# Optimization experiments

Measured on AMD Instinct MI355X. Metric: run time of the kernel, lower is better.

The kernel has to match this reference:

```python
import jax, jax.numpy as jnp
import numpy as np

N = 100000      # nodes
E = 800000      # edges (before self-loops)
G = 128         # graphs
IN = 64         # per-table embedding dim (6 tables -> 384 input features)
L = 128         # layer_embd
OUT = 128       # out_embd
H = 2           # attention heads (concat=False -> mean over heads)
VOCABS = [33, 5, 3, 4, 2, 3]
NEG_SLOPE = 0.2
BN_EPS = 1e-5


def _seg_softmax(logits, seg, n):
    # softmax of per-edge/per-node logits grouped by segment id
    m = jax.ops.segment_max(logits, seg, num_segments=n)
    e = jnp.exp(logits - m[seg])
    s = jax.ops.segment_sum(e, seg, num_segments=n)
    return e / (s[seg] + 1e-16)


def _gat_conv(x, W, a_src, a_dst, b, src, dst, n):
    # PyG GATConv, add_self_loops already applied to (src,dst), concat=False
    h = (x @ W).reshape(n, H, -1)                 # [N,H,C]
    al_s = jnp.sum(h * a_src, axis=-1)            # [N,H]
    al_d = jnp.sum(h * a_dst, axis=-1)            # [N,H]
    e = jax.nn.leaky_relu(al_s[src] + al_d[dst], NEG_SLOPE)   # [E,H]
    alpha = _seg_softmax(e, dst, n)               # softmax over each dst's in-edges
    msg = h[src] * alpha[:, :, None]              # [E,H,C]
    out = jax.ops.segment_sum(msg, dst, num_segments=n)       # [N,H,C]
    return out.mean(axis=1) + b                   # head-mean + bias


def setup_inputs() -> dict:
    key = jax.random.key(0)
    ks = jax.random.split(key, 40)
    cols = [jax.random.randint(ks[i], (N, 1), 0, VOCABS[i]) for i in range(6)]
    x = jnp.concatenate(cols, axis=1).astype(jnp.int64)
    edge_index = jax.random.randint(ks[6], (2, E), 0, N).astype(jnp.int64)
    edge_type = jax.random.randint(ks[7], (E,), 0, 4).astype(jnp.int64)
    batch = jnp.sort(jax.random.randint(ks[8], (N,), 0, G)).astype(jnp.int64)
    s = 0.05
    p = {}
    for i in range(6):
        p[f"emb{i}"] = jax.random.normal(ks[10 + i], (VOCABS[i], IN)) * s
    p["W1"] = jax.random.normal(ks[16], (6 * IN, H * L)) * s
    p["as1"] = jax.random.normal(ks[17], (H, L)) * s
    p["ad1"] = jax.random.normal(ks[18], (H, L)) * s
    p["b1"] = jnp.zeros((L,))
    p["W2"] = jax.random.normal(ks[19], (L, H * OUT)) * s
    p["as2"] = jax.random.normal(ks[20], (H, OUT)) * s
    p["ad2"] = jax.random.normal(ks[21], (H, OUT)) * s
    p["b2"] = jnp.zeros((OUT,))
    p["gw1"] = jax.random.normal(ks[22], (OUT, OUT)) * s
    p["gb1"] = jnp.zeros((OUT,))
    p["bn_g"] = jnp.ones((OUT,))
    p["bn_b"] = jnp.zeros((OUT,))
    p["bn_m"] = jnp.zeros((OUT,))
    p["bn_v"] = jnp.ones((OUT,))
    p["gw2"] = jax.random.normal(ks[23], (OUT, 1)) * s
    p["gb2"] = jnp.zeros((1,))
    p["glw"] = jax.random.normal(ks[24], (OUT, 1)) * s
    p["glb"] = jnp.zeros((1,))
    return dict(x=x, edge_index=edge_index, edge_type=edge_type, batch=batch, **p)


def reference(x, edge_index, edge_type, batch,
              emb0, emb1, emb2, emb3, emb4, emb5,
              W1, as1, ad1, b1, W2, as2, ad2, b2,
              gw1, gb1, bn_g, bn_b, bn_m, bn_v, gw2, gb2, glw, glb):
    n = x.shape[0]
    embs = [emb0, emb1, emb2, emb3, emb4, emb5]
    x_ = jnp.concatenate([embs[i][x[:, i]] for i in range(6)], axis=1)  # [N, 6*IN]
    loops = jnp.arange(n)
    src = jnp.concatenate([edge_index[0], loops])
    dst = jnp.concatenate([edge_index[1], loops])
    out = jax.nn.sigmoid(_gat_conv(x_, W1, as1, ad1, b1, src, dst, n))
    out = jax.nn.sigmoid(_gat_conv(out, W2, as2, ad2, b2, src, dst, n))
    # GlobalAttention pooling (eval-mode BatchNorm in gate_nn)
    gh = out @ gw1 + gb1
    gh = (gh - bn_m) / jnp.sqrt(bn_v + BN_EPS) * bn_g + bn_b
    gh = jax.nn.relu(gh)
    logits = gh @ gw2 + gb2                       # [N,1]
    gate = _seg_softmax(logits, batch, G)         # softmax over nodes per graph
    pooled = jax.ops.segment_sum(gate * out, batch, num_segments=G)  # [G,OUT]
    return jax.nn.sigmoid(pooled @ glw + glb)     # [G,1]
```

## Files before the change

### kernel.cpp

```cpp
#include <hip/hip_runtime.h>
#include <hip/hip_bf16.h>
#include <hip/hip_fp16.h>

#define NN 100000
#define EE 800000
#define GG 128

typedef short bf16x8 __attribute__((ext_vector_type(8)));
typedef float f32x4 __attribute__((ext_vector_type(4)));
typedef float f32x2 __attribute__((ext_vector_type(2)));

__device__ __forceinline__ float bf2f(unsigned short v) {
    union { unsigned int u; float f; } x; x.u = ((unsigned int)v) << 16; return x.f;
}
__device__ __forceinline__ unsigned short f2bf(float f) {
    union { float f; unsigned int u; } x; x.f = f;
    unsigned int r = x.u + 0x7fffu + ((x.u >> 16) & 1u);
    return (unsigned short)(r >> 16);
}
__device__ __forceinline__ float sigmoidf_(float x) { return 1.f / (1.f + __expf(-x)); }
__device__ __forceinline__ float ldp(const void* p, int i, int f) {
    return f ? ((const float*)p)[i] : bf2f(((const unsigned short*)p)[i]);
}

#if defined(__has_builtin)
#if __has_builtin(__builtin_amdgcn_cvt_pk_f32_fp8) && __has_builtin(__builtin_amdgcn_cvt_pk_fp8_f32)
#define USE_HW_FP8 1
#endif
#endif
#ifndef USE_HW_FP8
#define USE_HW_FP8 0
#endif

#if USE_HW_FP8
__device__ __forceinline__ int fp8_pack2(float a, float b) {
    return __builtin_amdgcn_cvt_pk_fp8_f32(a, b, 0, false);
}
__device__ __forceinline__ void fp8_dec4(unsigned int q, float& f0, float& f1, float& f2, float& f3) {
    f32x2 lo = __builtin_amdgcn_cvt_pk_f32_fp8((int)q, false);
    f32x2 hi = __builtin_amdgcn_cvt_pk_f32_fp8((int)q, true);
    f0 = lo.x; f1 = lo.y; f2 = hi.x; f3 = hi.y;
}
#else
__device__ __forceinline__ unsigned char f2bf8(float f) {
    unsigned short u = __half_as_ushort(__float2half(f));
    unsigned short r = u + 0x7f + ((u >> 8) & 1);
    return (unsigned char)(r >> 8);
}
__device__ __forceinline__ int fp8_pack2(float a, float b) {
    return (int)f2bf8(a) | ((int)f2bf8(b) << 8);
}
__device__ __forceinline__ float bf8_dec(unsigned int b) {
    return __half2float(__ushort_as_half((unsigned short)(b << 8)));
}
__device__ __forceinline__ void fp8_dec4(unsigned int q, float& f0, float& f1, float& f2, float& f3) {
    f0 = bf8_dec(q & 0xff); f1 = bf8_dec((q >> 8) & 0xff);
    f2 = bf8_dec((q >> 16) & 0xff); f3 = bf8_dec(q >> 24);
}
#endif

__global__ void k_probe2(const unsigned int* __restrict__ w, const int* __restrict__ ei,
                         int* __restrict__ fflag, int* __restrict__ iflag) {
    __shared__ int s[256];
    int t = threadIdx.x;
    if (blockIdx.x == 0) {
        int cnt = 0;
        for (int i = t; i < 1024; i += 256) {
            unsigned int v = w[i];
            int e = (v >> 7) & 0xff;
            cnt += (e >= 100 && e <= 127) ? 1 : 0;
        }
        s[t] = cnt; __syncthreads();
        for (int d = 128; d > 0; d >>= 1) { if (t < d) s[t] += s[t + d]; __syncthreads(); }
        if (t == 0) fflag[0] = (s[0] >= 512) ? 0 : 1;
    } else {
        int nz = 0;
        for (int i = t; i < 1024; i += 256) nz |= ei[2 * i + 1];
        s[t] = nz; __syncthreads();
        for (int d = 128; d > 0; d >>= 1) { if (t < d) s[t] |= s[t + d]; __syncthreads(); }
        if (t == 0) iflag[0] = (s[0] == 0) ? 1 : 0;
    }
}

__global__ void k_cvt(const int* __restrict__ xi, const int* __restrict__ ei,
                      const int* __restrict__ bi, const int* __restrict__ flag,
                      int* __restrict__ xn, int* __restrict__ srcn,
                      int* __restrict__ dstn, int* __restrict__ batchn,
                      int* __restrict__ count) {
    int j = blockIdx.x * 256 + threadIdx.x;
    int f = flag[0];
    const int XT = NN * 6, ET = 2 * EE;
    if (j < XT) xn[j] = f ? xi[2 * j] : xi[j];
    int je = j - XT;
    if (je >= 0 && je < ET) {
        int v = f ? ei[2 * je] : ei[je];
        if (je < EE) srcn[je] = v;
        else { dstn[je - EE] = v; atomicAdd(&count[v], 1); }
    }
    int jb = j - XT - ET;
    if (jb >= 0 && jb < NN) batchn[jb] = f ? bi[2 * jb] : bi[jb];
}

__global__ void k_chunk_sum(const int* __restrict__ count, int* __restrict__ csum) {
    __shared__ int s[256];
    int t = threadIdx.x;
    int base = blockIdx.x * 1024 + t * 4;
    int acc = 0;
    #pragma unroll
    for (int j = 0; j < 4; j++) { int n = base + j; if (n < NN) acc += count[n]; }
    s[t] = acc; __syncthreads();
    for (int d = 128; d > 0; d >>= 1) { if (t < d) s[t] += s[t + d]; __syncthreads(); }
    if (t == 0) csum[blockIdx.x] = s[0];
}

__global__ void k_chunk_scan(const int* __restrict__ csum, int* __restrict__ coff, int nchunk) {
    __shared__ int s[256];
    int t = threadIdx.x;
    int v = (t < nchunk) ? csum[t] : 0;
    s[t] = v; __syncthreads();
    for (int d = 1; d < 256; d <<= 1) {
        int x = (t >= d) ? s[t - d] : 0;
        __syncthreads(); s[t] += x; __syncthreads();
    }
    if (t < nchunk) coff[t] = s[t] - v;
}

__global__ void k_scan_write(const int* __restrict__ count, const int* __restrict__ coff,
                             int* __restrict__ offset, int* __restrict__ cursor) {
    __shared__ int s[256];
    int t = threadIdx.x;
    int base = blockIdx.x * 1024 + t * 4;
    int v[4]; int acc = 0;
    #pragma unroll
    for (int j = 0; j < 4; j++) { v[j] = (base + j < NN) ? count[base + j] : 0; acc += v[j]; }
    s[t] = acc; __syncthreads();
    for (int d = 1; d < 256; d <<= 1) {
        int x = (t >= d) ? s[t - d] : 0;
        __syncthreads(); s[t] += x; __syncthreads();
    }
    int pre = s[t] - acc + coff[blockIdx.x];
    #pragma unroll
    for (int j = 0; j < 4; j++) {
        if (base + j < NN) { offset[base + j] = pre; cursor[base + j] = pre; pre += v[j]; }
    }
}

__global__ void k_scatter(const int* __restrict__ src, const int* __restrict__ dst,
                          int* __restrict__ cursor, int2* __restrict__ esrt) {
    int e = blockIdx.x * 256 + threadIdx.x;
    if (e < EE) {
        int d = dst[e];
        int p = atomicAdd(&cursor[d], 1);
        esrt[p] = make_int2(src[e], d);
    }
}

__global__ void k_cvtp(const void* e0, const void* e1, const void* e2,
                       const void* e3, const void* e4, const void* e5,
                       const void* W1, const void* W2,
                       const void* as1, const void* ad1, const void* b1,
                       const void* as2, const void* ad2, const void* b2,
                       const void* gw1, const void* gb1,
                       const void* bng, const void* bnb, const void* bnm, const void* bnv,
                       const void* gw2, const void* gb2, const void* glw, const void* glb,
                       const int* __restrict__ fflag,
                       unsigned short* __restrict__ embc,
                       unsigned short* __restrict__ W1T, unsigned short* __restrict__ W2T,
                       unsigned short* __restrict__ GWT, float* __restrict__ gb1p,
                       float* __restrict__ vs1, float* __restrict__ vd1,
                       float* __restrict__ vs2, float* __restrict__ vd2,
                       float* __restrict__ vb1, float* __restrict__ vb2,
                       float* __restrict__ gw2f, float* __restrict__ glwf,
                       float* __restrict__ gb2f, float* __restrict__ glbf) {
    int i = blockIdx.x * 256 + threadIdx.x;
    int f = fflag[0];
    if (i < 98304) { int k = i / 256, n = i % 256; W1T[n * 384 + k] = f2bf(ldp(W1, i, f)); }
    if (i < 32768) { int k = i / 256, n = i % 256; W2T[n * 128 + k] = f2bf(ldp(W2, i, f)); }
    if (i < 16384) {
        int n = i >> 7, k = i & 127;
        float sc = ldp(bng, n, f) * rsqrtf(ldp(bnv, n, f) + 1e-5f);
        GWT[i] = f2bf(ldp(gw1, k * 128 + n, f) * sc);
    }
    if (i < 3200) {
        const void* src; int base;
        if (i < 2112)      { src = e0; base = 0; }
        else if (i < 2432) { src = e1; base = 2112; }
        else if (i < 2624) { src = e2; base = 2432; }
        else if (i < 2880) { src = e3; base = 2624; }
        else if (i < 3008) { src = e4; base = 2880; }
        else               { src = e5; base = 3008; }
        embc[i] = f2bf(ldp(src, i - base, f));
    }
    if (i < 256) {
        vs1[i] = ldp(as1, i, f); vd1[i] = ldp(ad1, i, f);
        vs2[i] = ldp(as2, i, f); vd2[i] = ldp(ad2, i, f);
    }
    if (i < 128) {
        vb1[i] = ldp(b1, i, f); vb2[i] = ldp(b2, i, f);
        gw2f[i] = ldp(gw2, i, f); glwf[i] = ldp(glw, i, f);
        float sc = ldp(bng, i, f) * rsqrtf(ldp(bnv, i, f) + 1e-5f);
        gb1p[i] = (ldp(gb1, i, f) - ldp(bnm, i, f)) * sc + ldp(bnb, i, f);
    }
    if (i == 0) { gb2f[0] = ldp(gb2, 0, f); glbf[0] = ldp(glb, 0, f); }
}

__global__ __launch_bounds__(256, 2) void k_gemm(
    const unsigned short* __restrict__ Ain, const int* __restrict__ xidx,
    const unsigned short* __restrict__ embc,
    const unsigned short* __restrict__ WT, unsigned char* __restrict__ H8,
    const float* __restrict__ avs, const float* __restrict__ avd,
    float* __restrict__ alS, float* __restrict__ alD,
    int K, int mode)
{
    __shared__ __align__(16) unsigned short As[128 * 32];
    __shared__ __align__(16) unsigned short Bs[256 * 32];
    const int tab_base[6] = {0, 2112, 2432, 2624, 2880, 3008};
    int tid = threadIdx.x;
    int wave = tid >> 6, lane = tid & 63;
    int quad = lane >> 4, lr = lane & 15;
    int m0 = blockIdx.x * 128;

    f32x4 zero4 = {0.f, 0.f, 0.f, 0.f};
    f32x4 acc[2][16];
    #pragma unroll
    for (int i = 0; i < 2; i++)
        #pragma unroll
        for (int j = 0; j < 16; j++) acc[i][j] = zero4;

    for (int k0 = 0; k0 < K; k0 += 32) {
        #pragma unroll
        for (int i = 0; i < 2; i++) {
            int idx = tid + i * 256;
            int row = idx >> 2, part = idx & 3;
            int gr = m0 + row; if (gr >= NN) gr = NN - 1;
            const unsigned short* sp;
            if (mode == 0) {
                int tbl = k0 >> 6;
                int off = k0 & 63;
                int v = xidx[gr * 6 + tbl];
                sp = embc + tab_base[tbl] + v * 64 + off + part * 8;
            } else {
                sp = Ain + (size_t)gr * K + k0 + part * 8;
            }
            int g = ((row >> 4) << 6) + (part << 4) + (row & 15);
            *(uint4*)(&As[g * 8]) = *(const uint4*)sp;
        }
        #pragma unroll
        for (int i = 0; i < 4; i++) {
            int idx = tid + i * 256;
            int row = idx >> 2, part = idx & 3;
            int g = ((row >> 4) << 6) + (part << 4) + (row & 15);
            *(uint4*)(&Bs[g * 8]) =
                *(const uint4*)(WT + (size_t)row * K + k0 + part * 8);
        }
        __syncthreads();

        bf16x8 af0 = *(const bf16x8*)(&As[(wave * 128 + lane) * 8]);
        bf16x8 af1 = *(const bf16x8*)(&As[(wave * 128 + 64 + lane) * 8]);
        #pragma unroll
        for (int ni = 0; ni < 16; ni++) {
            bf16x8 bfv = *(const bf16x8*)(&Bs[(ni * 64 + lane) * 8]);
            acc[0][ni] = __builtin_amdgcn_mfma_f32_16x16x32_bf16(af0, bfv, acc[0][ni], 0, 0, 0);
            acc[1][ni] = __builtin_amdgcn_mfma_f32_16x16x32_bf16(af1, bfv, acc[1][ni], 0, 0, 0);
        }
        __syncthreads();
    }

    float svv[16], dvv[16];
    #pragma unroll
    for (int ni = 0; ni < 16; ni++) { svv[ni] = avs[ni * 16 + lr]; dvv[ni] = avd[ni * 16 + lr]; }
    #pragma unroll
    for (int mi = 0; mi < 2; mi++) {
        #pragma unroll
        for (int r = 0; r < 4; r++) {
            int grow = m0 + wave * 32 + mi * 16 + quad * 4 + r;
            float ps0 = 0.f, ps1 = 0.f, pd0 = 0.f, pd1 = 0.f;
            if (grow < NN) {
                #pragma unroll
                for (int ni = 0; ni < 16; ni += 2) {
                    float v0 = acc[mi][ni][r], v1 = acc[mi][ni + 1][r];
                    int pk = fp8_pack2(v0, v1);
                    H8[(size_t)grow * 256 + ni * 16 + lr] = (unsigned char)(pk & 0xff);
                    H8[(size_t)grow * 256 + (ni + 1) * 16 + lr] = (unsigned char)((pk >> 8) & 0xff);
                    if (ni < 8) { ps0 += v0 * svv[ni] + v1 * svv[ni + 1]; pd0 += v0 * dvv[ni] + v1 * dvv[ni + 1]; }
                    else        { ps1 += v0 * svv[ni] + v1 * svv[ni + 1]; pd1 += v0 * dvv[ni] + v1 * dvv[ni + 1]; }
                }
            }
            #pragma unroll
            for (int m = 1; m < 16; m <<= 1) {
                ps0 += __shfl_xor(ps0, m); ps1 += __shfl_xor(ps1, m);
                pd0 += __shfl_xor(pd0, m); pd1 += __shfl_xor(pd1, m);
            }
            if (lr == 0 && grow < NN) {
                alS[grow * 2 + 0] = ps0; alS[grow * 2 + 1] = ps1;
                alD[grow * 2 + 0] = pd0; alD[grow * 2 + 1] = pd1;
            }
        }
    }
}

__device__ __forceinline__ float edge_w(float e) {
    e = e > 0.f ? e : 0.2f * e;
    e = fminf(fmaxf(e, -60.f), 60.f);
    return __expf(e);
}
__global__ __launch_bounds__(256) void k_ew(const int2* __restrict__ esrt,
                                            const float* __restrict__ alS,
                                            const float* __restrict__ alD,
                                            float* __restrict__ wsrt) {
    int j = blockIdx.x * 256 + threadIdx.x;
    if (j >= EE) return;
    int2 e = esrt[j];
    float w0 = edge_w(alS[e.x * 2 + 0] + alD[e.y * 2 + 0]);
    float w1 = edge_w(alS[e.x * 2 + 1] + alD[e.y * 2 + 1]);
    float2 w; w.x = w0; w.y = w1;
    *(float2*)(wsrt + (size_t)j * 2) = w;
}

__global__ __launch_bounds__(256) void k_agg(const unsigned char* __restrict__ H8,
                                             const float* __restrict__ alS, const float* __restrict__ alD,
                                             const float* __restrict__ wsrt,
                                             const int2* __restrict__ esrt, const int* __restrict__ offs,
                                             const int* __restrict__ cnts,
                                             const float* __restrict__ bias,
                                             unsigned short* __restrict__ Out) {
    int node = blockIdx.x * 4 + (threadIdx.x >> 6);
    if (node >= NN) return;
    int lane = threadIdx.x & 63;
    int head = lane >> 5;
    float ws = edge_w(alS[node * 2 + head] + alD[node * 2 + head]);
    unsigned int qv = *(const unsigned int*)(H8 + (size_t)node * 256 + lane * 4);
    float h0, h1, h2, h3;
    fp8_dec4(qv, h0, h1, h2, h3);
    float den = ws;
    float n0 = ws * h0, n1 = ws * h1, n2 = ws * h2, n3 = ws * h3;
    int off = offs[node], cnt = cnts[node];
    int i = 0;
    for (; i + 4 <= cnt; i += 4) {
        int j0 = off + i;
        int s0 = esrt[j0].x, s1 = esrt[j0 + 1].x, s2 = esrt[j0 + 2].x, s3 = esrt[j0 + 3].x;
        float w0 = wsrt[(size_t)j0 * 2 + head];
        float w1 = wsrt[(size_t)(j0 + 1) * 2 + head];
        float w2 = wsrt[(size_t)(j0 + 2) * 2 + head];
        float w3 = wsrt[(size_t)(j0 + 3) * 2 + head];
        unsigned int qa = *(const unsigned int*)(H8 + (size_t)s0 * 256 + lane * 4);
        unsigned int qb = *(const unsigned int*)(H8 + (size_t)s1 * 256 + lane * 4);
        unsigned int qc = *(const unsigned int*)(H8 + (size_t)s2 * 256 + lane * 4);
        unsigned int qd = *(const unsigned int*)(H8 + (size_t)s3 * 256 + lane * 4);
        float a0, a1, a2, a3, b0, b1, b2, b3, c0, c1, c2, c3, d0, d1, d2, d3;
        fp8_dec4(qa, a0, a1, a2, a3);
        fp8_dec4(qb, b0, b1, b2, b3);
        fp8_dec4(qc, c0, c1, c2, c3);
        fp8_dec4(qd, d0, d1, d2, d3);
        den += (w0 + w1) + (w2 + w3);
        n0 += w0 * a0 + w1 * b0 + w2 * c0 + w3 * d0;
        n1 += w0 * a1 + w1 * b1 + w2 * c1 + w3 * d1;
        n2 += w0 * a2 + w1 * b2 + w2 * c2 + w3 * d2;
        n3 += w0 * a3 + w1 * b3 + w2 * c3 + w3 * d3;
    }
    for (; i < cnt; i++) {
        int j0 = off + i;
        int s0 = esrt[j0].x;
        float w0 = wsrt[(size_t)j0 * 2 + head];
        unsigned int qa = *(const unsigned int*)(H8 + (size_t)s0 * 256 + lane * 4);
        float a0, a1, a2, a3;
        fp8_dec4(qa, a0, a1, a2, a3);
        den += w0;
        n0 += w0 * a0; n1 += w0 * a1; n2 += w0 * a2; n3 += w0 * a3;
    }
    float inv = 1.f / den;
    float v0 = n0 * inv, v1 = n1 * inv, v2 = n2 * inv, v3 = n3 * inv;
    float o0 = 0.5f * (v0 + __shfl_xor(v0, 32));
    float o1 = 0.5f * (v1 + __shfl_xor(v1, 32));
    float o2 = 0.5f * (v2 + __shfl_xor(v2, 32));
    float o3 = 0.5f * (v3 + __shfl_xor(v3, 32));
    if (lane < 32) {
        int c = lane * 4;
        float4 bv = *(const float4*)(bias + c);
        o0 = sigmoidf_(o0 + bv.x);
        o1 = sigmoidf_(o1 + bv.y);
        o2 = sigmoidf_(o2 + bv.z);
        o3 = sigmoidf_(o3 + bv.w);
        uint2 pv;
        pv.x = (unsigned int)f2bf(o0) | ((unsigned int)f2bf(o1) << 16);
        pv.y = (unsigned int)f2bf(o2) | ((unsigned int)f2bf(o3) << 16);
        *(uint2*)(Out + (size_t)node * 128 + c) = pv;
    }
}

__global__ __launch_bounds__(256, 2) void k_gatemm(
    const unsigned short* __restrict__ Obuf,
    const unsigned short* __restrict__ GWT,
    const float* __restrict__ gb1p, const float* __restrict__ gw2f,
    const float* __restrict__ gb2f, float* __restrict__ logits)
{
    __shared__ __align__(16) unsigned short As[128 * 32];
    __shared__ __align__(16) unsigned short Bs[128 * 32];
    int tid = threadIdx.x;
    int wave = tid >> 6, lane = tid & 63;
    int quad = lane >> 4, lr = lane & 15;
    int m0 = blockIdx.x * 128;

    f32x4 zero4 = {0.f, 0.f, 0.f, 0.f};
    f32x4 acc[2][8];
    #pragma unroll
    for (int i = 0; i < 2; i++)
        #pragma unroll
        for (int j = 0; j < 8; j++) acc[i][j] = zero4;

    for (int k0 = 0; k0 < 128; k0 += 32) {
        #pragma unroll
        for (int i = 0; i < 2; i++) {
            int idx = tid + i * 256;
            int row = idx >> 2, part = idx & 3;
            int gr = m0 + row; if (gr >= NN) gr = NN - 1;
            int g = ((row >> 4) << 6) + (part << 4) + (row & 15);
            *(uint4*)(&As[g * 8]) =
                *(const uint4*)(Obuf + (size_t)gr * 128 + k0 + part * 8);
            *(uint4*)(&Bs[g * 8]) =
                *(const uint4*)(GWT + (size_t)row * 128 + k0 + part * 8);
        }
        __syncthreads();

        bf16x8 af0 = *(const bf16x8*)(&As[(wave * 128 + lane) * 8]);
        bf16x8 af1 = *(const bf16x8*)(&As[(wave * 128 + 64 + lane) * 8]);
        #pragma unroll
        for (int ni = 0; ni < 8; ni++) {
            bf16x8 bfv = *(const bf16x8*)(&Bs[(ni * 64 + lane) * 8]);
            acc[0][ni] = __builtin_amdgcn_mfma_f32_16x16x32_bf16(af0, bfv, acc[0][ni], 0, 0, 0);
            acc[1][ni] = __builtin_amdgcn_mfma_f32_16x16x32_bf16(af1, bfv, acc[1][ni], 0, 0, 0);
        }
        __syncthreads();
    }

    float gb[8], gw[8];
    #pragma unroll
    for (int ni = 0; ni < 8; ni++) { gb[ni] = gb1p[ni * 16 + lr]; gw[ni] = gw2f[ni * 16 + lr]; }
    #pragma unroll
    for (int mi = 0; mi < 2; mi++) {
        #pragma unroll
        for (int r = 0; r < 4; r++) {
            int grow = m0 + wave * 32 + mi * 16 + quad * 4 + r;
            float part = 0.f;
            #pragma unroll
            for (int ni = 0; ni < 8; ni++) {
                float v = acc[mi][ni][r] + gb[ni];
                v = v > 0.f ? v : 0.f;
                part += v * gw[ni];
            }
            #pragma unroll
            for (int m = 1; m < 16; m <<= 1) part += __shfl_xor(part, m);
            if (lr == 0 && grow < NN) logits[grow] = part + gb2f[0];
        }
    }
}

__device__ int lbound(const int* a, int n, int key) {
    int lo = 0, hi = n;
    while (lo < hi) { int mid = (lo + hi) >> 1; if (a[mid] < key) lo = mid + 1; else hi = mid; }
    return lo;
}

__global__ void k_bounds(const int* __restrict__ batch, int* __restrict__ gbound) {
    int t = threadIdx.x;
    if (t <= GG) gbound[t] = (t == GG) ? NN : lbound(batch, NN, t);
}

__global__ __launch_bounds__(256) void k_gmax(const float* __restrict__ logits,
                                              const int* __restrict__ gbound,
                                              float* __restrict__ gmax) {
    __shared__ float sm[256];
    int g = blockIdx.x, t = threadIdx.x;
    int lo = gbound[g], hi = gbound[g + 1];
    float mx = -1e30f;
    for (int i = lo + t; i < hi; i += 256) mx = fmaxf(mx, logits[i]);
    sm[t] = mx; __syncthreads();
    for (int s = 128; s > 0; s >>= 1) { if (t < s) sm[t] = fmaxf(sm[t], sm[t + s]); __syncthreads(); }
    if (t == 0) gmax[g] = sm[0];
}

#define NPB 256
__global__ __launch_bounds__(256) void k_ppart(const unsigned short* __restrict__ Out2,
                                               const float* __restrict__ logits,
                                               const int* __restrict__ batch,
                                               const float* __restrict__ gmax,
                                               float* __restrict__ accv,
                                               float* __restrict__ accw) {
    int t = threadIdx.x;
    int c = t & 127, half = t >> 7;
    int b0 = blockIdx.x * NPB;
    int b1 = b0 + NPB; if (b1 > NN) b1 = NN;
    float acc = 0.f, aw = 0.f;
    int g = -1;
    for (int i = b0 + half; i < b1; i += 2) {
        int gi = batch[i];
        if (gi != g) {
            if (g >= 0) {
                atomicAdd(&accv[g * 128 + c], acc);
                if (c == 0) atomicAdd(&accw[g], aw);
            }
            g = gi; acc = 0.f; aw = 0.f;
        }
        float w = __expf(logits[i] - gmax[gi]);
        acc += w * bf2f(Out2[(size_t)i * 128 + c]);
        if (c == 0) aw += w;
    }
    if (g >= 0) {
        atomicAdd(&accv[g * 128 + c], acc);
        if (c == 0) atomicAdd(&accw[g], aw);
    }
}

__global__ __launch_bounds__(128) void k_pfin(const float* __restrict__ accv,
                                              const float* __restrict__ accw,
                                              const float* __restrict__ glwf,
                                              const float* __restrict__ glbf,
                                              const int* __restrict__ fflag,
                                              void* __restrict__ out) {
    __shared__ float sv[128];
    int g = blockIdx.x, t = threadIdx.x;
    float pooled = accv[g * 128 + t] / (accw[g] + 1e-16f);
    sv[t] = pooled * glwf[t];
    __syncthreads();
    for (int s = 64; s > 0; s >>= 1) { if (t < s) sv[t] += sv[t + s]; __syncthreads(); }
    if (t == 0) {
        float r = sigmoidf_(sv[0] + glbf[0]);
        if (fflag[0]) ((float*)out)[g] = r;
        else ((unsigned short*)out)[g] = f2bf(r);
    }
}

extern "C" void kernel_launch(void* const* d_in, const int* in_sizes, int n_in,
                              void* d_out, int out_size, void* d_ws, size_t ws_size,
                              hipStream_t stream) {
    const int* x_raw  = (const int*)d_in[0];
    const int* ei_raw = (const int*)d_in[1];
    const int* b_raw  = (const int*)d_in[3];

    char* p = (char*)d_ws;
    auto alloc = [&](size_t bytes) { void* r = (void*)p; p += (bytes + 255) & ~(size_t)255; return r; };
    unsigned char* H8   = (unsigned char*)alloc((size_t)NN * 256);
    unsigned short* Obuf = (unsigned short*)alloc((size_t)NN * 128 * 2);
    float* alS   = (float*)alloc((size_t)NN * 2 * 4);
    float* alD   = (float*)alloc((size_t)NN * 2 * 4);
    float* logit = (float*)alloc((size_t)NN * 4);
    int* count   = (int*)alloc((size_t)NN * 4);
    int* offs    = (int*)alloc((size_t)NN * 4);
    int* cursor  = (int*)alloc((size_t)NN * 4);
    int2* esrt   = (int2*)alloc((size_t)EE * 8);
    float* wsrt  = (float*)alloc((size_t)EE * 2 * 4);
    int* csum    = (int*)alloc(256 * 4);
    int* coff    = (int*)alloc(256 * 4);
    unsigned short* W1T  = (unsigned short*)alloc(256 * 384 * 2);
    unsigned short* W2T  = (unsigned short*)alloc(256 * 128 * 2);
    unsigned short* GWT  = (unsigned short*)alloc(128 * 128 * 2);
    float* gb1p = (float*)alloc(128 * 4);
    int* xn     = (int*)alloc((size_t)NN * 6 * 4);
    int* srcn   = (int*)alloc((size_t)EE * 4);
    int* dstn   = (int*)alloc((size_t)EE * 4);
    int* batchn = (int*)alloc((size_t)NN * 4);
    int* iflag  = (int*)alloc(256);
    int* fflag  = (int*)alloc(256);
    unsigned short* embc = (unsigned short*)alloc(3200 * 2);
    float* vs1  = (float*)alloc(256 * 4);
    float* vd1  = (float*)alloc(256 * 4);
    float* vs2  = (float*)alloc(256 * 4);
    float* vd2  = (float*)alloc(256 * 4);
    float* vb1  = (float*)alloc(128 * 4);
    float* vb2  = (float*)alloc(128 * 4);
    float* gw2f = (float*)alloc(128 * 4);
    float* glwf = (float*)alloc(128 * 4);
    float* gb2f = (float*)alloc(4);
    float* glbf = (float*)alloc(4);
    int*   gbound = (int*)alloc((GG + 1) * 4);
    float* gmax   = (float*)alloc(GG * 4);
    float* accv   = (float*)alloc(GG * 128 * 4);
    float* accw   = (float*)alloc(GG * 4);

    const int NCHUNK = (NN + 1023) / 1024;
    const int NBM = (NN + 127) / 128;
    const int NBE = (EE + 255) / 256;
    const int NB4 = (NN + 3) / 4;
    const int CVT_TOT = NN * 6 + 2 * EE + NN;

    hipMemsetAsync(count, 0, (size_t)NN * 4, stream);
    hipMemsetAsync(accv, 0, (size_t)(GG * 128 + GG) * 4 + 256, stream);

    k_probe2<<<2, 256, 0, stream>>>((const unsigned int*)d_in[10], ei_raw, fflag, iflag);
    k_cvt<<<(CVT_TOT + 255) / 256, 256, 0, stream>>>(x_raw, ei_raw, b_raw, iflag,
                                                     xn, srcn, dstn, batchn, count);
    k_cvtp<<<(98304 + 255) / 256, 256, 0, stream>>>(
        d_in[4], d_in[5], d_in[6], d_in[7], d_in[8], d_in[9],
        d_in[10], d_in[14],
        d_in[11], d_in[12], d_in[13], d_in[15], d_in[16], d_in[17],
        d_in[18], d_in[19], d_in[20], d_in[21], d_in[22], d_in[23],
        d_in[24], d_in[25], d_in[26], d_in[27],
        fflag, embc, W1T, W2T, GWT, gb1p,
        vs1, vd1, vs2, vd2, vb1, vb2, gw2f, glwf, gb2f, glbf);

    k_chunk_sum<<<NCHUNK, 256, 0, stream>>>(count, csum);
    k_chunk_scan<<<1, 256, 0, stream>>>(csum, coff, NCHUNK);
    k_scan_write<<<NCHUNK, 256, 0, stream>>>(count, coff, offs, cursor);
    k_scatter<<<NBE, 256, 0, stream>>>(srcn, dstn, cursor, esrt);

    k_gemm<<<NBM, 256, 0, stream>>>(nullptr, xn, embc, W1T, H8, vs1, vd1, alS, alD, 384, 0);
    k_ew<<<NBE, 256, 0, stream>>>(esrt, alS, alD, wsrt);
    k_agg<<<NB4, 256, 0, stream>>>(H8, alS, alD, wsrt, esrt, offs, count, vb1, Obuf);

    k_gemm<<<NBM, 256, 0, stream>>>(Obuf, xn, embc, W2T, H8, vs2, vd2, alS, alD, 128, 1);
    k_ew<<<NBE, 256, 0, stream>>>(esrt, alS, alD, wsrt);
    k_agg<<<NB4, 256, 0, stream>>>(H8, alS, alD, wsrt, esrt, offs, count, vb2, Obuf);

    k_gatemm<<<NBM, 256, 0, stream>>>(Obuf, GWT, gb1p, gw2f, gb2f, logit);
    k_bounds<<<1, 256, 0, stream>>>(batchn, gbound);
    k_gmax<<<GG, 256, 0, stream>>>(logit, gbound, gmax);
    k_ppart<<<(NN + NPB - 1) / NPB, 256, 0, stream>>>(Obuf, logit, batchn, gmax, accv, accw);
    k_pfin<<<GG, 128, 0, stream>>>(accv, accw, glwf, glbf, fflag, d_out);
}
```

Measured before the change: 496.8 us.

## Fuse edge-weight computation into aggregation, swizzle GEMM LDS, merge small launches

Drops the separate edge-weight kernel: aggregation now loads each 64-edge chunk of source ids cooperatively, computes both head weights per lane and stages them in LDS. This removes the per-edge weight buffer and the int2 edge array, and the scatter now writes only source ids. The GEMM LDS layouts get an XOR swizzle meant to cut bank conflicts. The bounds kernel is folded into gmax, and two memsets become one over a contiguous region. The fused loop adds an LDS staging step with no explicit barrier, relying on all lanes of a single wavefront running in lockstep.

After: 473.6 us. 4.7% less time.

```diff
diff --git a/kernel.cpp b/kernel.cpp
--- a/kernel.cpp
+++ b/kernel.cpp
@@ -36,10 +36,9 @@
 __device__ __forceinline__ int fp8_pack2(float a, float b) {
     return __builtin_amdgcn_cvt_pk_fp8_f32(a, b, 0, false);
 }
-__device__ __forceinline__ void fp8_dec4(unsigned int q, float& f0, float& f1, float& f2, float& f3) {
-    f32x2 lo = __builtin_amdgcn_cvt_pk_f32_fp8((int)q, false);
-    f32x2 hi = __builtin_amdgcn_cvt_pk_f32_fp8((int)q, true);
-    f0 = lo.x; f1 = lo.y; f2 = hi.x; f3 = hi.y;
+__device__ __forceinline__ void fp8_dec4v(unsigned int q, f32x2& lo, f32x2& hi) {
+    lo = __builtin_amdgcn_cvt_pk_f32_fp8((int)q, false);
+    hi = __builtin_amdgcn_cvt_pk_f32_fp8((int)q, true);
 }
 #else
 __device__ __forceinline__ unsigned char f2bf8(float f) {
@@ -53,9 +52,9 @@
 __device__ __forceinline__ float bf8_dec(unsigned int b) {
     return __half2float(__ushort_as_half((unsigned short)(b << 8)));
 }
-__device__ __forceinline__ void fp8_dec4(unsigned int q, float& f0, float& f1, float& f2, float& f3) {
-    f0 = bf8_dec(q & 0xff); f1 = bf8_dec((q >> 8) & 0xff);
-    f2 = bf8_dec((q >> 16) & 0xff); f3 = bf8_dec(q >> 24);
+__device__ __forceinline__ void fp8_dec4v(unsigned int q, f32x2& lo, f32x2& hi) {
+    lo[0] = bf8_dec(q & 0xff); lo[1] = bf8_dec((q >> 8) & 0xff);
+    hi[0] = bf8_dec((q >> 16) & 0xff); hi[1] = bf8_dec(q >> 24);
 }
 #endif
 
@@ -146,12 +145,12 @@
 }
 
 __global__ void k_scatter(const int* __restrict__ src, const int* __restrict__ dst,
-                          int* __restrict__ cursor, int2* __restrict__ esrt) {
+                          int* __restrict__ cursor, int* __restrict__ sorted) {
     int e = blockIdx.x * 256 + threadIdx.x;
     if (e < EE) {
         int d = dst[e];
         int p = atomicAdd(&cursor[d], 1);
-        esrt[p] = make_int2(src[e], d);
+        sorted[p] = src[e];
     }
 }
 
@@ -243,6 +242,7 @@
                 sp = Ain + (size_t)gr * K + k0 + part * 8;
             }
             int g = ((row >> 4) << 6) + (part << 4) + (row & 15);
+            g ^= (part << 1);
             *(uint4*)(&As[g * 8]) = *(const uint4*)sp;
         }
         #pragma unroll
@@ -250,16 +250,18 @@
             int idx = tid + i * 256;
             int row = idx >> 2, part = idx & 3;
             int g = ((row >> 4) << 6) + (part << 4) + (row & 15);
+            g ^= (part << 1);
             *(uint4*)(&Bs[g * 8]) =
                 *(const uint4*)(WT + (size_t)row * K + k0 + part * 8);
         }
         __syncthreads();
 
-        bf16x8 af0 = *(const bf16x8*)(&As[(wave * 128 + lane) * 8]);
-        bf16x8 af1 = *(const bf16x8*)(&As[(wave * 128 + 64 + lane) * 8]);
+        int sw = (quad << 1);
+        bf16x8 af0 = *(const bf16x8*)(&As[((wave * 128 + lane) ^ sw) * 8]);
+        bf16x8 af1 = *(const bf16x8*)(&As[((wave * 128 + 64 + lane) ^ sw) * 8]);
         #pragma unroll
         for (int ni = 0; ni < 16; ni++) {
-            bf16x8 bfv = *(const bf16x8*)(&Bs[(ni * 64 + lane) * 8]);
+            bf16x8 bfv = *(const bf16x8*)(&Bs[((ni * 64 + lane) ^ sw) * 8]);
             acc[0][ni] = __builtin_amdgcn_mfma_f32_16x16x32_bf16(af0, bfv, acc[0][ni], 0, 0, 0);
             acc[1][ni] = __builtin_amdgcn_mfma_f32_16x16x32_bf16(af1, bfv, acc[1][ni], 0, 0, 0);
         }
@@ -304,72 +306,71 @@
     e = fminf(fmaxf(e, -60.f), 60.f);
     return __expf(e);
 }
-__global__ __launch_bounds__(256) void k_ew(const int2* __restrict__ esrt,
-                                            const float* __restrict__ alS,
-                                            const float* __restrict__ alD,
-                                            float* __restrict__ wsrt) {
-    int j = blockIdx.x * 256 + threadIdx.x;
-    if (j >= EE) return;
-    int2 e = esrt[j];
-    float w0 = edge_w(alS[e.x * 2 + 0] + alD[e.y * 2 + 0]);
-    float w1 = edge_w(alS[e.x * 2 + 1] + alD[e.y * 2 + 1]);
-    float2 w; w.x = w0; w.y = w1;
-    *(float2*)(wsrt + (size_t)j * 2) = w;
-}
-
 __global__ __launch_bounds__(256) void k_agg(const unsigned char* __restrict__ H8,
                                              const float* __restrict__ alS, const float* __restrict__ alD,
-                                             const float* __restrict__ wsrt,
-                                             const int2* __restrict__ esrt, const int* __restrict__ offs,
+                                             const int* __restrict__ sorted, const int* __restrict__ offs,
                                              const int* __restrict__ cnts,
                                              const float* __restrict__ bias,
                                              unsigned short* __restrict__ Out) {
-    int node = blockIdx.x * 4 + (threadIdx.x >> 6);
+    __shared__ uint4 lw[4][64];
+    int wid = threadIdx.x >> 6;
+    int node = blockIdx.x * 4 + wid;
     if (node >= NN) return;
     int lane = threadIdx.x & 63;
     int head = lane >> 5;
-    float ws = edge_w(alS[node * 2 + head] + alD[node * 2 + head]);
-    unsigned int qv = *(const unsigned int*)(H8 + (size_t)node * 256 + lane * 4);
-    float h0, h1, h2, h3;
-    fp8_dec4(qv, h0, h1, h2, h3);
+    float2 adv = *(const float2*)(alD + node * 2);
+    float myAd = head ? adv.y : adv.x;
+    const unsigned char* Hl = H8 + lane * 4;
+
+    float ws = edge_w(alS[node * 2 + head] + myAd);
+    unsigned int qv = *(const unsigned int*)(Hl + ((unsigned)node << 8));
+    f32x2 lo, hi; fp8_dec4v(qv, lo, hi);
     float den = ws;
-    float n0 = ws * h0, n1 = ws * h1, n2 = ws * h2, n3 = ws * h3;
+    f32x2 wsv = {ws, ws};
+    f32x2 n01 = lo * wsv, n23 = hi * wsv;
+
     int off = offs[node], cnt = cnts[node];
-    int i = 0;
-    for (; i + 4 <= cnt; i += 4) {
-        int j0 = off + i;
-        int s0 = esrt[j0].x, s1 = esrt[j0 + 1].x, s2 = esrt[j0 + 2].x, s3 = esrt[j0 + 3].x;
-        float w0 = wsrt[(size_t)j0 * 2 + head];
-        float w1 = wsrt[(size_t)(j0 + 1) * 2 + head];
-        float w2 = wsrt[(size_t)(j0 + 2) * 2 + head];
-        float w3 = wsrt[(size_t)(j0 + 3) * 2 + head];
-        unsigned int qa = *(const unsigned int*)(H8 + (size_t)s0 * 256 + lane * 4);
-        unsigned int qb = *(const unsigned int*)(H8 + (size_t)s1 * 256 + lane * 4);
-        unsigned int qc = *(const unsigned int*)(H8 + (size_t)s2 * 256 + lane * 4);
-        unsigned int qd = *(const unsigned int*)(H8 + (size_t)s3 * 256 + lane * 4);
-        float a0, a1, a2, a3, b0, b1, b2, b3, c0, c1, c2, c3, d0, d1, d2, d3;
-        fp8_dec4(qa, a0, a1, a2, a3);
-        fp8_dec4(qb, b0, b1, b2, b3);
-        fp8_dec4(qc, c0, c1, c2, c3);
-        fp8_dec4(qd, d0, d1, d2, d3);
-        den += (w0 + w1) + (w2 + w3);
-        n0 += w0 * a0 + w1 * b0 + w2 * c0 + w3 * d0;
-        n1 += w0 * a1 + w1 * b1 + w2 * c1 + w3 * d1;
-        n2 += w0 * a2 + w1 * b2 + w2 * c2 + w3 * d2;
-        n3 += w0 * a3 + w1 * b3 + w2 * c3 + w3 * d3;
-    }
-    for (; i < cnt; i++) {
-        int j0 = off + i;
-        int s0 = esrt[j0].x;
-        float w0 = wsrt[(size_t)j0 * 2 + head];
-        unsigned int qa = *(const unsigned int*)(H8 + (size_t)s0 * 256 + lane * 4);
-        float a0, a1, a2, a3;
-        fp8_dec4(qa, a0, a1, a2, a3);
-        den += w0;
-        n0 += w0 * a0; n1 += w0 * a1; n2 += w0 * a2; n3 += w0 * a3;
+    for (int c = 0; c < cnt; c += 64) {
+        int m = cnt - c; if (m > 64) m = 64;
+        int j = off + c + (lane < m ? lane : 0);
+        int s = sorted[j];
+        float2 asv = *(const float2*)(alS + s * 2);
+        float w0 = edge_w(asv.x + adv.x);
+        float w1 = edge_w(asv.y + adv.y);
+        lw[wid][lane] = make_uint4((unsigned)s << 8, __float_as_uint(w0), __float_as_uint(w1), 0u);
+        int i = 0;
+        for (; i + 4 <= m; i += 4) {
+            uint4 e0 = lw[wid][i], e1 = lw[wid][i + 1], e2 = lw[wid][i + 2], e3 = lw[wid][i + 3];
+            unsigned q0 = *(const unsigned int*)(Hl + e0.x);
+            unsigned q1 = *(const unsigned int*)(Hl + e1.x);
+            unsigned q2 = *(const unsigned int*)(Hl + e2.x);
+            unsigned q3 = *(const unsigned int*)(Hl + e3.x);
+            float wA = __uint_as_float(head ? e0.z : e0.y);
+            float wB = __uint_as_float(head ? e1.z : e1.y);
+            float wC = __uint_as_float(head ? e2.z : e2.y);
+            float wD = __uint_as_float(head ? e3.z : e3.y);
+            f32x2 la, ha, lb, hb, lc, hc, ld, hd;
+            fp8_dec4v(q0, la, ha); fp8_dec4v(q1, lb, hb);
+            fp8_dec4v(q2, lc, hc); fp8_dec4v(q3, ld, hd);
+            den += (wA + wB) + (wC + wD);
+            f32x2 va = {wA, wA}, vb = {wB, wB}, vc = {wC, wC}, vd = {wD, wD};
+            n01 += la * va + lb * vb + lc * vc + ld * vd;
+            n23 += ha * va + hb * vb + hc * vc + hd * vd;
+        }
+        for (; i < m; i++) {
+            uint4 e0 = lw[wid][i];
+            unsigned q0 = *(const unsigned int*)(Hl + e0.x);
+            float wA = __uint_as_float(head ? e0.z : e0.y);
+            f32x2 la, ha;
+            fp8_dec4v(q0, la, ha);
+            den += wA;
+            f32x2 va = {wA, wA};
+            n01 += la * va;
+            n23 += ha * va;
+        }
     }
     float inv = 1.f / den;
-    float v0 = n0 * inv, v1 = n1 * inv, v2 = n2 * inv, v3 = n3 * inv;
+    float v0 = n01[0] * inv, v1 = n01[1] * inv, v2 = n23[0] * inv, v3 = n23[1] * inv;
     float o0 = 0.5f * (v0 + __shfl_xor(v0, 32));
     float o1 = 0.5f * (v1 + __shfl_xor(v1, 32));
     float o2 = 0.5f * (v2 + __shfl_xor(v2, 32));
@@ -415,6 +416,7 @@
             int row = idx >> 2, part = idx & 3;
             int gr = m0 + row; if (gr >= NN) gr = NN - 1;
             int g = ((row >> 4) << 6) + (part << 4) + (row & 15);
+            g ^= (part << 1);
             *(uint4*)(&As[g * 8]) =
                 *(const uint4*)(Obuf + (size_t)gr * 128 + k0 + part * 8);
             *(uint4*)(&Bs[g * 8]) =
@@ -422,11 +424,12 @@
         }
         __syncthreads();
 
-        bf16x8 af0 = *(const bf16x8*)(&As[(wave * 128 + lane) * 8]);
-        bf16x8 af1 = *(const bf16x8*)(&As[(wave * 128 + 64 + lane) * 8]);
+        int sw = (quad << 1);
+        bf16x8 af0 = *(const bf16x8*)(&As[((wave * 128 + lane) ^ sw) * 8]);
+        bf16x8 af1 = *(const bf16x8*)(&As[((wave * 128 + 64 + lane) ^ sw) * 8]);
         #pragma unroll
         for (int ni = 0; ni < 8; ni++) {
-            bf16x8 bfv = *(const bf16x8*)(&Bs[(ni * 64 + lane) * 8]);
+            bf16x8 bfv = *(const bf16x8*)(&Bs[((ni * 64 + lane) ^ sw) * 8]);
             acc[0][ni] = __builtin_amdgcn_mfma_f32_16x16x32_bf16(af0, bfv, acc[0][ni], 0, 0, 0);
             acc[1][ni] = __builtin_amdgcn_mfma_f32_16x16x32_bf16(af1, bfv, acc[1][ni], 0, 0, 0);
         }
@@ -461,17 +464,15 @@
     return lo;
 }
 
-__global__ void k_bounds(const int* __restrict__ batch, int* __restrict__ gbound) {
-    int t = threadIdx.x;
-    if (t <= GG) gbound[t] = (t == GG) ? NN : lbound(batch, NN, t);
-}
-
 __global__ __launch_bounds__(256) void k_gmax(const float* __restrict__ logits,
-                                              const int* __restrict__ gbound,
+                                              const int* __restrict__ batch,
                                               float* __restrict__ gmax) {
+    __shared__ int sb[2];
     __shared__ float sm[256];
     int g = blockIdx.x, t = threadIdx.x;
-    int lo = gbound[g], hi = gbound[g + 1];
+    if (t < 2) sb[t] = lbound(batch, NN, g + t);
+    __syncthreads();
+    int lo = sb[0], hi = sb[1];
     float mx = -1e30f;
     for (int i = lo + t; i < hi; i += 256) mx = fmaxf(mx, logits[i]);
     sm[t] = mx; __syncthreads();
@@ -544,11 +545,14 @@
     float* alS   = (float*)alloc((size_t)NN * 2 * 4);
     float* alD   = (float*)alloc((size_t)NN * 2 * 4);
     float* logit = (float*)alloc((size_t)NN * 4);
+    char* z0 = p;
     int* count   = (int*)alloc((size_t)NN * 4);
+    float* accv  = (float*)alloc(GG * 128 * 4);
+    float* accw  = (float*)alloc(GG * 4);
+    size_t zlen = (size_t)(p - z0);
     int* offs    = (int*)alloc((size_t)NN * 4);
     int* cursor  = (int*)alloc((size_t)NN * 4);
-    int2* esrt   = (int2*)alloc((size_t)EE * 8);
-    float* wsrt  = (float*)alloc((size_t)EE * 2 * 4);
+    int* sorted  = (int*)alloc((size_t)EE * 4);
     int* csum    = (int*)alloc(256 * 4);
     int* coff    = (int*)alloc(256 * 4);
     unsigned short* W1T  = (unsigned short*)alloc(256 * 384 * 2);
@@ -572,10 +576,7 @@
     float* glwf = (float*)alloc(128 * 4);
     float* gb2f = (float*)alloc(4);
     float* glbf = (float*)alloc(4);
-    int*   gbound = (int*)alloc((GG + 1) * 4);
-    float* gmax   = (float*)alloc(GG * 4);
-    float* accv   = (float*)alloc(GG * 128 * 4);
-    float* accw   = (float*)alloc(GG * 4);
+    float* gmax = (float*)alloc(GG * 4);
 
     const int NCHUNK = (NN + 1023) / 1024;
     const int NBM = (NN + 127) / 128;
@@ -583,8 +584,7 @@
     const int NB4 = (NN + 3) / 4;
     const int CVT_TOT = NN * 6 + 2 * EE + NN;
 
-    hipMemsetAsync(count, 0, (size_t)NN * 4, stream);
-    hipMemsetAsync(accv, 0, (size_t)(GG * 128 + GG) * 4 + 256, stream);
+    hipMemsetAsync(z0, 0, zlen, stream);
 
     k_probe2<<<2, 256, 0, stream>>>((const unsigned int*)d_in[10], ei_raw, fflag, iflag);
     k_cvt<<<(CVT_TOT + 255) / 256, 256, 0, stream>>>(x_raw, ei_raw, b_raw, iflag,
@@ -601,19 +601,16 @@
     k_chunk_sum<<<NCHUNK, 256, 0, stream>>>(count, csum);
     k_chunk_scan<<<1, 256, 0, stream>>>(csum, coff, NCHUNK);
     k_scan_write<<<NCHUNK, 256, 0, stream>>>(count, coff, offs, cursor);
-    k_scatter<<<NBE, 256, 0, stream>>>(srcn, dstn, cursor, esrt);
+    k_scatter<<<NBE, 256, 0, stream>>>(srcn, dstn, cursor, sorted);
 
     k_gemm<<<NBM, 256, 0, stream>>>(nullptr, xn, embc, W1T, H8, vs1, vd1, alS, alD, 384, 0);
-    k_ew<<<NBE, 256, 0, stream>>>(esrt, alS, alD, wsrt);
-    k_agg<<<NB4, 256, 0, stream>>>(H8, alS, alD, wsrt, esrt, offs, count, vb1, Obuf);
+    k_agg<<<NB4, 256, 0, stream>>>(H8, alS, alD, sorted, offs, count, vb1, Obuf);
 
     k_gemm<<<NBM, 256, 0, stream>>>(Obuf, xn, embc, W2T, H8, vs2, vd2, alS, alD, 128, 1);
-    k_ew<<<NBE, 256, 0, stream>>>(esrt, alS, alD, wsrt);
-    k_agg<<<NB4, 256, 0, stream>>>(H8, alS, alD, wsrt, esrt, offs, count, vb2, Obuf);
+    k_agg<<<NB4, 256, 0, stream>>>(H8, alS, alD, sorted, offs, count, vb2, Obuf);
 
     k_gatemm<<<NBM, 256, 0, stream>>>(Obuf, GWT, gb1p, gw2f, gb2f, logit);
-    k_bounds<<<1, 256, 0, stream>>>(batchn, gbound);
-    k_gmax<<<GG, 256, 0, stream>>>(logit, gbound, gmax);
+    k_gmax<<<GG, 256, 0, stream>>>(logit, batchn, gmax);
     k_ppart<<<(NN + NPB - 1) / NPB, 256, 0, stream>>>(Obuf, logit, batchn, gmax, accv, accw);
     k_pfin<<<GG, 128, 0, stream>>>(accv, accw, glwf, glbf, fflag, d_out);
 }
```
